# Optimization experiments

Measured on AMD Instinct MI355X. Metric: run time of the kernel, lower is better.

## Reference

```python
import jax, jax.numpy as jnp
import numpy as np

NODE_DIM = 256
OUT_DIM = 512
NUM_HEADS = 8
HEAD_DIM = 32
HID = NUM_HEADS * HEAD_DIM  # 256
N_NODES = 200000
N_GRAPHS = 2000


def _linear_init(key, fan_in, fan_out):
    lim = 1.0 / np.sqrt(fan_in)
    kw, kb = jax.random.split(key)
    w = jax.random.uniform(kw, (fan_in, fan_out), minval=-lim, maxval=lim, dtype=jnp.float32)
    b = jax.random.uniform(kb, (fan_out,), minval=-lim, maxval=lim, dtype=jnp.float32)
    return w, b


def setup_inputs() -> dict:
    key = jax.random.key(0)
    ks = jax.random.split(key, 16)
    inp = {}
    inp["node_embeddings"] = jax.random.normal(ks[0], (N_NODES, NODE_DIM), dtype=jnp.float32)
    inp["node_to_graph_id"] = jnp.sort(jax.random.randint(ks[1], (N_NODES,), 0, N_GRAPHS)).astype(jnp.int64)
    inp["num_graphs"] = N_GRAPHS
    # weighted_mean pooler params
    inp["wm_score_w1"], inp["wm_score_b1"] = _linear_init(ks[2], NODE_DIM, HID)
    inp["wm_score_w2"], inp["wm_score_b2"] = _linear_init(ks[3], HID, NUM_HEADS)
    inp["wm_val_w1"], inp["wm_val_b1"] = _linear_init(ks[4], NODE_DIM, HID)
    inp["wm_val_w2"], inp["wm_val_b2"] = _linear_init(ks[5], HID, NUM_HEADS * HEAD_DIM)
    inp["wm_comb_w"] = _linear_init(ks[6], NUM_HEADS * HEAD_DIM, OUT_DIM)[0]
    # weighted_sum pooler params
    inp["ws_score_w1"], inp["ws_score_b1"] = _linear_init(ks[7], NODE_DIM, HID)
    inp["ws_score_w2"], inp["ws_score_b2"] = _linear_init(ks[8], HID, NUM_HEADS)
    inp["ws_val_w1"], inp["ws_val_b1"] = _linear_init(ks[9], NODE_DIM, HID)
    inp["ws_val_w2"], inp["ws_val_b2"] = _linear_init(ks[10], HID, NUM_HEADS * HEAD_DIM)
    inp["ws_comb_w"] = _linear_init(ks[11], NUM_HEADS * HEAD_DIM, OUT_DIM)[0]
    # max pooler + final combination
    inp["mx_comb_w"] = _linear_init(ks[12], NODE_DIM, OUT_DIM)[0]
    inp["final_w"] = _linear_init(ks[13], 3 * OUT_DIM, OUT_DIM)[0]
    return inp


def _mlp(x, w1, b1, w2, b2):
    return jax.nn.relu(x @ w1 + b1) @ w2 + b2


def _scatter_softmax(scores, seg, num_graphs):
    # scores: [N, H]; softmax over nodes within each graph, per head
    m = jax.ops.segment_max(scores, seg, num_segments=num_graphs)
    m = jnp.where(jnp.isfinite(m), m, 0.0)  # empty graphs
    e = jnp.exp(scores - m[seg])
    s = jax.ops.segment_sum(e, seg, num_segments=num_graphs)
    return e / s[seg]


def _multihead_readout(x, seg, num_graphs, sw1, sb1, sw2, sb2, vw1, vb1, vw2, vb2, cw, weighted_mean):
    scores = _mlp(x, sw1, sb1, sw2, sb2)                       # [N, heads]
    if weighted_mean:
        weights = _scatter_softmax(scores, seg, num_graphs)
    else:
        weights = jax.nn.sigmoid(scores)
    values = _mlp(x, vw1, vb1, vw2, vb2).reshape(-1, NUM_HEADS, HEAD_DIM)
    weighted = (weights[:, :, None] * values).reshape(-1, NUM_HEADS * HEAD_DIM)
    per_graph = jax.ops.segment_sum(weighted, seg, num_segments=num_graphs)
    return per_graph @ cw


def reference(node_embeddings, node_to_graph_id, num_graphs,
              wm_score_w1, wm_score_b1, wm_score_w2, wm_score_b2,
              wm_val_w1, wm_val_b1, wm_val_w2, wm_val_b2, wm_comb_w,
              ws_score_w1, ws_score_b1, ws_score_w2, ws_score_b2,
              ws_val_w1, ws_val_b1, ws_val_w2, ws_val_b2, ws_comb_w,
              mx_comb_w, final_w):
    seg = node_to_graph_id.astype(jnp.int32)
    mean_repr = _multihead_readout(node_embeddings, seg, num_graphs,
                                   wm_score_w1, wm_score_b1, wm_score_w2, wm_score_b2,
                                   wm_val_w1, wm_val_b1, wm_val_w2, wm_val_b2, wm_comb_w, True)
    sum_repr = _multihead_readout(node_embeddings, seg, num_graphs,
                                  ws_score_w1, ws_score_b1, ws_score_w2, ws_score_b2,
                                  ws_val_w1, ws_val_b1, ws_val_w2, ws_val_b2, ws_comb_w, False)
    pg_max = jax.ops.segment_max(node_embeddings, seg, num_segments=num_graphs)
    pg_max = jnp.where(jnp.isfinite(pg_max), pg_max, 0.0)  # torch_scatter zeros empty segments
    max_repr = pg_max @ mx_comb_w
    raw = jnp.concatenate([mean_repr, sum_repr, max_repr], axis=1)  # [G, 3*out_dim]
    return jax.nn.relu(raw) @ final_w
```

## Files before the change

### kernel.cpp

```cpp
#include <hip/hip_runtime.h>
#include <hip/hip_bf16.h>

typedef __bf16 bf16_t;
typedef __bf16 bf16x8 __attribute__((ext_vector_type(8)));
typedef float  f32x4  __attribute__((ext_vector_type(4)));

#define MFMA16(a, b, c) __builtin_amdgcn_mfma_f32_16x16x32_bf16((a), (b), (c), 0, 0, 0)

#define ROWS 32

__device__ __forceinline__ int gray(int row) { return (row ^ (row >> 1)) & 7; }
__device__ __forceinline__ int swz256(int row, int col) {
    return row * 256 + ((((col >> 3) ^ gray(row)) << 3) | (col & 7));
}

__device__ __forceinline__ bf16x8 cvt8(float4 a, float4 b) {
    bf16x8 o;
    o[0] = (bf16_t)a.x; o[1] = (bf16_t)a.y; o[2] = (bf16_t)a.z; o[3] = (bf16_t)a.w;
    o[4] = (bf16_t)b.x; o[5] = (bf16_t)b.y; o[6] = (bf16_t)b.z; o[7] = (bf16_t)b.w;
    return o;
}

__device__ __forceinline__ unsigned enc_max(float x) {
    unsigned b = __float_as_uint(x);
    return (b & 0x80000000u) ? ~b : (b | 0x80000000u);
}
__device__ __forceinline__ float dec_max(unsigned e) {
    if (e == 0u) return 0.0f;
    return (e & 0x80000000u) ? __uint_as_float(e ^ 0x80000000u) : __uint_as_float(~e);
}

__device__ __forceinline__ void gemm256p(const bf16_t* __restrict__ As,
                                         const bf16_t* __restrict__ Wk,
                                         f32x4 acc[2][2], int w, int l) {
    const int l15 = l & 15, hi = l >> 4;
#pragma unroll
    for (int mt = 0; mt < 2; ++mt)
#pragma unroll
        for (int j = 0; j < 2; ++j) acc[mt][j] = (f32x4){0.f, 0.f, 0.f, 0.f};

    const bf16_t* wb = Wk + ((size_t)hi * 256 + w * 32 + l15) * 8;

    bf16x8 b0[3], b1[3];
    bf16x8 a[2][2];
    b0[0] = *(const bf16x8*)(wb);
    b1[0] = *(const bf16x8*)(wb + 128);
    b0[1] = *(const bf16x8*)(wb + 8192);
    b1[1] = *(const bf16x8*)(wb + 8192 + 128);
#pragma unroll
    for (int mt = 0; mt < 2; ++mt) {
        const int row = mt * 16 + l15;
        a[0][mt] = *(const bf16x8*)(As + row * 256 + (hi ^ gray(row)) * 8);
    }

#pragma unroll
    for (int kt = 0; kt < 8; ++kt) {
        const int cur = kt % 3, nx2 = (kt + 2) % 3;
        if (kt + 2 < 8) {
            b0[nx2] = *(const bf16x8*)(wb + (kt + 2) * 8192);
            b1[nx2] = *(const bf16x8*)(wb + (kt + 2) * 8192 + 128);
        }
        if (kt + 1 < 8) {
#pragma unroll
            for (int mt = 0; mt < 2; ++mt) {
                const int row = mt * 16 + l15;
                a[(kt + 1) & 1][mt] =
                    *(const bf16x8*)(As + row * 256 + (((kt + 1) * 4 + hi) ^ gray(row)) * 8);
            }
        }
#pragma unroll
        for (int mt = 0; mt < 2; ++mt) {
            acc[mt][0] = MFMA16(a[kt & 1][mt], b0[cur], acc[mt][0]);
            acc[mt][1] = MFMA16(a[kt & 1][mt], b1[cur], acc[mt][1]);
        }
    }
}

__device__ __forceinline__ void write_h(f32x4 acc[2][2], const float* __restrict__ bias,
                                        bool relu, bf16_t* __restrict__ dst, int w, int l) {
    const int l15 = l & 15, hi = l >> 4;
#pragma unroll
    for (int j = 0; j < 2; ++j) {
        const int col = w * 32 + j * 16 + l15;
        const float bv = bias[col];
#pragma unroll
        for (int mt = 0; mt < 2; ++mt)
#pragma unroll
            for (int r = 0; r < 4; ++r) {
                const int row = mt * 16 + hi * 4 + r;
                float v = acc[mt][j][r] + bv;
                if (relu) v = fmaxf(v, 0.f);
                dst[swz256(row, col)] = (bf16_t)v;
            }
    }
}

__device__ __forceinline__ void gemm_score(const bf16_t* __restrict__ As,
                                           const bf16_t* __restrict__ W2k,
                                           const float* __restrict__ b2,
                                           float* __restrict__ ssc, int coloff, int w, int l) {
    if (w >= 2) return;
    const int l15 = l & 15, hi = l >> 4;
    const int row = w * 16 + l15;
    const bf16_t* wb = W2k + ((size_t)hi * 16 + l15) * 8;
    bf16x8 b[3];
    b[0] = *(const bf16x8*)(wb);
    b[1] = *(const bf16x8*)(wb + 512);
    f32x4 acc = (f32x4){0.f, 0.f, 0.f, 0.f};
#pragma unroll
    for (int kt = 0; kt < 8; ++kt) {
        const int cur = kt % 3, nx2 = (kt + 2) % 3;
        if (kt + 2 < 8) b[nx2] = *(const bf16x8*)(wb + (kt + 2) * 512);
        bf16x8 a = *(const bf16x8*)(As + row * 256 + ((kt * 4 + hi) ^ gray(row)) * 8);
        acc = MFMA16(a, b[cur], acc);
    }
    if (l15 < 8) {
        const float bv = b2[l15];
#pragma unroll
        for (int r = 0; r < 4; ++r) {
            const int orow = w * 16 + hi * 4 + r;
            ssc[orow * 16 + coloff + l15] = acc[r] + bv;
        }
    }
}

template <bool WM>
__device__ __forceinline__ void reduce_seg(const bf16_t* __restrict__ sh,
                                           const float* __restrict__ ssc,
                                           const bf16_t* __restrict__ sx,
                                           const int* __restrict__ sseg,
                                           float* __restrict__ num, float* __restrict__ den,
                                           unsigned* __restrict__ pmax, int G) {
    const int col = threadIdx.x & 255;
    const int rbeg = (threadIdx.x >> 8) * 16;
    float av = 0.f, ad = 0.f;
    unsigned am = 0u;
    int gcur = sseg[rbeg];
    for (int r = rbeg; r < rbeg + 16; ++r) {
        const int g = sseg[r];
        if (g != gcur) {
            if ((unsigned)gcur < (unsigned)G) {
                atomicAdd(&num[(size_t)gcur * 256 + col], av);
                if (WM) {
                    if (col < 8) atomicAdd(&den[(size_t)gcur * 8 + col], ad);
                    atomicMax(&pmax[(size_t)gcur * 256 + col], am);
                }
            }
            av = 0.f; ad = 0.f; am = 0u; gcur = g;
        }
        const int si = swz256(r, col);
        const float v = (float)sh[si];
        const float wgt = ssc[r * 16 + (WM ? 0 : 8) + (col >> 5)];
        av += wgt * v;
        if (WM) {
            if (col < 8) ad += ssc[r * 16 + col];
            am = max(am, enc_max((float)sx[si]));
        }
    }
    if ((unsigned)gcur < (unsigned)G) {
        atomicAdd(&num[(size_t)gcur * 256 + col], av);
        if (WM) {
            if (col < 8) atomicAdd(&den[(size_t)gcur * 8 + col], ad);
            atomicMax(&pmax[(size_t)gcur * 256 + col], am);
        }
    }
}

__global__ __launch_bounds__(512, 3) void node_kernel(
    const float* __restrict__ X, const int* __restrict__ seg,
    const bf16_t* __restrict__ wt_sw1_wm, const bf16_t* __restrict__ wt_sw2_wm,
    const bf16_t* __restrict__ wt_vw1_wm, const bf16_t* __restrict__ wt_vw2_wm,
    const bf16_t* __restrict__ wt_sw1_ws, const bf16_t* __restrict__ wt_sw2_ws,
    const bf16_t* __restrict__ wt_vw1_ws, const bf16_t* __restrict__ wt_vw2_ws,
    const float* __restrict__ b_sw1_wm, const float* __restrict__ b_sw2_wm,
    const float* __restrict__ b_vw1_wm, const float* __restrict__ b_vw2_wm,
    const float* __restrict__ b_sw1_ws, const float* __restrict__ b_sw2_ws,
    const float* __restrict__ b_vw1_ws, const float* __restrict__ b_vw2_ws,
    float* __restrict__ num_wm, float* __restrict__ den_wm,
    float* __restrict__ acc_ws, unsigned* __restrict__ pmax, int N, int G) {
    __shared__ __align__(16) bf16_t sx[ROWS * 256];
    __shared__ __align__(16) bf16_t sh[ROWS * 256];
    __shared__ float ssc[ROWS * 16];
    __shared__ int sseg[ROWS];

    const int tid = threadIdx.x;
    const int w = tid >> 6, l = tid & 63;
    const int r0 = blockIdx.x * ROWS;

#pragma unroll
    for (int i = 0; i < 2; ++i) {
        const int cid = tid + i * 512;
        const int row = cid >> 5, ch = cid & 31;
        bf16x8 o;
        if (r0 + row < N) {
            const float4* gp = (const float4*)(X + (size_t)(r0 + row) * 256 + ch * 8);
            o = cvt8(gp[0], gp[1]);
        } else {
            for (int j = 0; j < 8; ++j) o[j] = (bf16_t)0.f;
        }
        *(bf16x8*)(sx + row * 256 + (ch ^ gray(row)) * 8) = o;
    }
    if (tid < ROWS) sseg[tid] = (r0 + tid < N) ? seg[r0 + tid] : -1;
    __syncthreads();

    f32x4 acc[2][2];

    gemm256p(sx, wt_sw1_wm, acc, w, l);
    write_h(acc, b_sw1_wm, true, sh, w, l);
    __syncthreads();
    gemm_score(sh, wt_sw2_wm, b_sw2_wm, ssc, 0, w, l);
    __syncthreads();

    gemm256p(sx, wt_sw1_ws, acc, w, l);
    write_h(acc, b_sw1_ws, true, sh, w, l);
    __syncthreads();
    gemm_score(sh, wt_sw2_ws, b_sw2_ws, ssc, 8, w, l);
    __syncthreads();

    {
        const float v = ssc[tid];
        ssc[tid] = ((tid & 15) < 8) ? __expf(v) : 1.f / (1.f + __expf(-v));
    }
    __syncthreads();

    gemm256p(sx, wt_vw1_wm, acc, w, l);
    write_h(acc, b_vw1_wm, true, sh, w, l);
    __syncthreads();
    gemm256p(sh, wt_vw2_wm, acc, w, l);
    __syncthreads();
    write_h(acc, b_vw2_wm, false, sh, w, l);
    __syncthreads();
    reduce_seg<true>(sh, ssc, sx, sseg, num_wm, den_wm, pmax, G);
    __syncthreads();

    gemm256p(sx, wt_vw1_ws, acc, w, l);
    write_h(acc, b_vw1_ws, true, sh, w, l);
    __syncthreads();
    gemm256p(sh, wt_vw2_ws, acc, w, l);
    __syncthreads();
    write_h(acc, b_vw2_ws, false, sx, w, l);
    __syncthreads();
    reduce_seg<false>(sx, ssc, sx, sseg, acc_ws, nullptr, nullptr, G);
}

__global__ __launch_bounds__(256, 2) void graph_kernel(
    const float* __restrict__ num_wm, const float* __restrict__ den_wm,
    const float* __restrict__ acc_ws, const unsigned* __restrict__ pmax,
    const bf16_t* __restrict__ wt_comb_wm, const bf16_t* __restrict__ wt_comb_ws,
    const bf16_t* __restrict__ wt_comb_mx, const bf16_t* __restrict__ wt_final,
    float* __restrict__ out, int G) {
    __shared__ __align__(16) bf16_t sa[16 * 256];
    __shared__ __align__(16) bf16_t sraw[16 * 1536];

    const int tid = threadIdx.x, w = tid >> 6, l = tid & 63;
    const int l15 = l & 15, hi = l >> 4;
    const int g0 = blockIdx.x * 16;

    for (int src = 0; src < 3; ++src) {
#pragma unroll
        for (int i = 0; i < 2; ++i) {
            const int cid = tid + i * 256;
            const int row = cid >> 5, ch = cid & 31;
            const int g = g0 + row;
            bf16x8 o;
            if (g < G) {
                if (src == 0) {
                    const float4* np = (const float4*)(num_wm + (size_t)g * 256 + ch * 8);
                    float4 v0 = np[0], v1 = np[1];
                    const float d = den_wm[(size_t)g * 8 + (ch >> 2)];
                    const float rd = (d > 0.f) ? 1.f / d : 0.f;
                    o[0] = (bf16_t)(v0.x * rd); o[1] = (bf16_t)(v0.y * rd);
                    o[2] = (bf16_t)(v0.z * rd); o[3] = (bf16_t)(v0.w * rd);
                    o[4] = (bf16_t)(v1.x * rd); o[5] = (bf16_t)(v1.y * rd);
                    o[6] = (bf16_t)(v1.z * rd); o[7] = (bf16_t)(v1.w * rd);
                } else if (src == 1) {
                    const float4* np = (const float4*)(acc_ws + (size_t)g * 256 + ch * 8);
                    o = cvt8(np[0], np[1]);
                } else {
                    const unsigned* mp = pmax + (size_t)g * 256 + ch * 8;
#pragma unroll
                    for (int j = 0; j < 8; ++j) o[j] = (bf16_t)dec_max(mp[j]);
                }
            } else {
                for (int j = 0; j < 8; ++j) o[j] = (bf16_t)0.f;
            }
            *(bf16x8*)(sa + row * 256 + (ch ^ gray(row)) * 8) = o;
        }
        __syncthreads();

        const bf16_t* Wt = (src == 0) ? wt_comb_wm : ((src == 1) ? wt_comb_ws : wt_comb_mx);
        bf16x8 a[8];
#pragma unroll
        for (int kt = 0; kt < 8; ++kt)
            a[kt] = *(const bf16x8*)(sa + l15 * 256 + ((kt * 4 + hi) ^ gray(l15)) * 8);
        f32x4 acc[8];
#pragma unroll
        for (int j = 0; j < 8; ++j) acc[j] = (f32x4){0.f, 0.f, 0.f, 0.f};
#pragma unroll
        for (int kt = 0; kt < 8; ++kt) {
            bf16x8 b[8];
#pragma unroll
            for (int j = 0; j < 8; ++j) {
                const int ncol = (w * 8 + j) * 16 + l15;
                b[j] = *(const bf16x8*)(Wt + ((size_t)(kt * 4 + hi) * 512 + ncol) * 8);
            }
#pragma unroll
            for (int j = 0; j < 8; ++j) acc[j] = MFMA16(a[kt], b[j], acc[j]);
        }
#pragma unroll
        for (int j = 0; j < 8; ++j) {
            const int col = src * 512 + (w * 8 + j) * 16 + l15;
#pragma unroll
            for (int r = 0; r < 4; ++r) {
                const int row = hi * 4 + r;
                const float v = fmaxf(acc[j][r], 0.f);
                sraw[row * 1536 + ((((col >> 3) ^ gray(row)) << 3) | (col & 7))] = (bf16_t)v;
            }
        }
        __syncthreads();
    }

    f32x4 facc[8];
#pragma unroll
    for (int j = 0; j < 8; ++j) facc[j] = (f32x4){0.f, 0.f, 0.f, 0.f};
    for (int kt = 0; kt < 48; ++kt) {
        bf16x8 a = *(const bf16x8*)(sraw + l15 * 1536 + ((kt * 4 + hi) ^ gray(l15)) * 8);
#pragma unroll
        for (int j = 0; j < 8; ++j) {
            const int ncol = (w * 8 + j) * 16 + l15;
            bf16x8 b = *(const bf16x8*)(wt_final + ((size_t)(kt * 4 + hi) * 512 + ncol) * 8);
            facc[j] = MFMA16(a, b, facc[j]);
        }
    }
#pragma unroll
    for (int j = 0; j < 8; ++j) {
        const int col = (w * 8 + j) * 16 + l15;
#pragma unroll
        for (int r = 0; r < 4; ++r) {
            const int row = hi * 4 + r;
            if (g0 + row < G) out[(size_t)(g0 + row) * 512 + col] = facc[j][r];
        }
    }
}

struct PrepTab {
    const float* src[12];
    bf16_t* dst[12];
    int K[12], Nn[12], Nout[12];
    int base[13];
};

__global__ void prep_all(PrepTab t) {
    const int idx = blockIdx.x * blockDim.x + threadIdx.x;
    if (idx >= t.base[12]) return;
    int i = 0;
#pragma unroll
    for (int s = 0; s < 12; ++s)
        if (idx >= t.base[s + 1]) i = s + 1;
    const int local = idx - t.base[i];
    const int j = local & 7;
    const int rest = local >> 3;
    const int n = rest % t.Nout[i];
    const int kc = rest / t.Nout[i];
    const int k = kc * 8 + j;
    const float v = (n < t.Nn[i]) ? t.src[i][(size_t)k * t.Nn[i] + n] : 0.f;
    t.dst[i][local] = (bf16_t)v;
}

extern "C" void kernel_launch(void* const* d_in, const int* in_sizes, int n_in,
                              void* d_out, int out_size, void* d_ws, size_t ws_size,
                              hipStream_t stream) {
    const float* X = (const float*)d_in[0];
    const int* seg = (const int*)d_in[1];
    const int N = in_sizes[1];
    const int G = out_size / 512;

    float* num_wm = (float*)d_ws;
    float* acc_ws = num_wm + (size_t)G * 256;
    float* den_wm = acc_ws + (size_t)G * 256;
    unsigned* pmax = (unsigned*)(den_wm + (size_t)G * 8);
    bf16_t* wt = (bf16_t*)(pmax + (size_t)G * 256);

    bf16_t* wt_sw1_wm = wt;
    bf16_t* wt_sw2_wm = wt_sw1_wm + 65536;
    bf16_t* wt_vw1_wm = wt_sw2_wm + 4096;
    bf16_t* wt_vw2_wm = wt_vw1_wm + 65536;
    bf16_t* wt_sw1_ws = wt_vw2_wm + 65536;
    bf16_t* wt_sw2_ws = wt_sw1_ws + 65536;
    bf16_t* wt_vw1_ws = wt_sw2_ws + 4096;
    bf16_t* wt_vw2_ws = wt_vw1_ws + 65536;
    bf16_t* wt_comb_wm = wt_vw2_ws + 65536;
    bf16_t* wt_comb_ws = wt_comb_wm + 131072;
    bf16_t* wt_comb_mx = wt_comb_ws + 131072;
    bf16_t* wt_final = wt_comb_mx + 131072;

    const size_t accum_bytes = ((size_t)G * 256 * 3 + (size_t)G * 8) * 4;
    hipMemsetAsync(d_ws, 0, accum_bytes, stream);

    struct TT { int srcIdx; bf16_t* dst; int K, Nn, Nout; };
    const TT tt[12] = {
        {3,  wt_sw1_wm, 256, 256, 256},  {5,  wt_sw2_wm, 256, 8,   16},
        {7,  wt_vw1_wm, 256, 256, 256},  {9,  wt_vw2_wm, 256, 256, 256},
        {12, wt_sw1_ws, 256, 256, 256},  {14, wt_sw2_ws, 256, 8,   16},
        {16, wt_vw1_ws, 256, 256, 256},  {18, wt_vw2_ws, 256, 256, 256},
        {11, wt_comb_wm, 256, 512, 512}, {20, wt_comb_ws, 256, 512, 512},
        {21, wt_comb_mx, 256, 512, 512}, {22, wt_final, 1536, 512, 512},
    };
    PrepTab pt;
    int base = 0;
    for (int i = 0; i < 12; ++i) {
        pt.src[i] = (const float*)d_in[tt[i].srcIdx];
        pt.dst[i] = tt[i].dst;
        pt.K[i] = tt[i].K; pt.Nn[i] = tt[i].Nn; pt.Nout[i] = tt[i].Nout;
        pt.base[i] = base;
        base += tt[i].K * tt[i].Nout;
    }
    pt.base[12] = base;
    prep_all<<<(base + 255) / 256, 256, 0, stream>>>(pt);

    const int nb = (N + ROWS - 1) / ROWS;
    node_kernel<<<nb, 512, 0, stream>>>(
        X, seg,
        wt_sw1_wm, wt_sw2_wm, wt_vw1_wm, wt_vw2_wm,
        wt_sw1_ws, wt_sw2_ws, wt_vw1_ws, wt_vw2_ws,
        (const float*)d_in[4], (const float*)d_in[6], (const float*)d_in[8], (const float*)d_in[10],
        (const float*)d_in[13], (const float*)d_in[15], (const float*)d_in[17], (const float*)d_in[19],
        num_wm, den_wm, acc_ws, pmax, N, G);

    const int gb = (G + 15) / 16;
    graph_kernel<<<gb, 256, 0, stream>>>(num_wm, den_wm, acc_ws, pmax,
                                         wt_comb_wm, wt_comb_ws, wt_comb_mx, wt_final,
                                         (float*)d_out, G);
}
```

Baseline: 325.6 us.

## Fuse value-MLP epilogue with segment reduction in registers and enlarge row tile

Replaces the write-to-LDS-then-reduce path for the value MLP outputs with a register-level reduction: each lane scales its MFMA accumulators by the softmax/sigmoid weight, sums per graph id via masked accumulation and cross-lane shuffles, and issues atomics directly. The rows per block grow from 32 to 48, so each block amortises its weight loads over more rows. The max pooling and the denominator accumulation are split into separate simpler passes. This removes two barriers and an LDS round-trip per pooler. In exchange, per-thread register pressure rises under a 3-blocks-per-CU launch bound, and the per-graph loop with shuffles runs once for every distinct graph id in the tile.

```diff
diff --git a/kernel.cpp b/kernel.cpp
--- a/kernel.cpp
+++ b/kernel.cpp
@@ -7,7 +7,7 @@
 
 #define MFMA16(a, b, c) __builtin_amdgcn_mfma_f32_16x16x32_bf16((a), (b), (c), 0, 0, 0)
 
-#define ROWS 32
+#define ROWS 48
 
 __device__ __forceinline__ int gray(int row) { return (row ^ (row >> 1)) & 7; }
 __device__ __forceinline__ int swz256(int row, int col) {
@@ -32,23 +32,23 @@
 
 __device__ __forceinline__ void gemm256p(const bf16_t* __restrict__ As,
                                          const bf16_t* __restrict__ Wk,
-                                         f32x4 acc[2][2], int w, int l) {
+                                         f32x4 acc[3][2], int w, int l) {
     const int l15 = l & 15, hi = l >> 4;
 #pragma unroll
-    for (int mt = 0; mt < 2; ++mt)
+    for (int mt = 0; mt < 3; ++mt)
 #pragma unroll
         for (int j = 0; j < 2; ++j) acc[mt][j] = (f32x4){0.f, 0.f, 0.f, 0.f};
 
     const bf16_t* wb = Wk + ((size_t)hi * 256 + w * 32 + l15) * 8;
 
     bf16x8 b0[3], b1[3];
-    bf16x8 a[2][2];
+    bf16x8 a[2][3];
     b0[0] = *(const bf16x8*)(wb);
     b1[0] = *(const bf16x8*)(wb + 128);
     b0[1] = *(const bf16x8*)(wb + 8192);
     b1[1] = *(const bf16x8*)(wb + 8192 + 128);
 #pragma unroll
-    for (int mt = 0; mt < 2; ++mt) {
+    for (int mt = 0; mt < 3; ++mt) {
         const int row = mt * 16 + l15;
         a[0][mt] = *(const bf16x8*)(As + row * 256 + (hi ^ gray(row)) * 8);
     }
@@ -62,36 +62,83 @@
         }
         if (kt + 1 < 8) {
 #pragma unroll
-            for (int mt = 0; mt < 2; ++mt) {
+            for (int mt = 0; mt < 3; ++mt) {
                 const int row = mt * 16 + l15;
                 a[(kt + 1) & 1][mt] =
                     *(const bf16x8*)(As + row * 256 + (((kt + 1) * 4 + hi) ^ gray(row)) * 8);
             }
         }
 #pragma unroll
-        for (int mt = 0; mt < 2; ++mt) {
+        for (int mt = 0; mt < 3; ++mt) {
             acc[mt][0] = MFMA16(a[kt & 1][mt], b0[cur], acc[mt][0]);
             acc[mt][1] = MFMA16(a[kt & 1][mt], b1[cur], acc[mt][1]);
         }
     }
 }
 
-__device__ __forceinline__ void write_h(f32x4 acc[2][2], const float* __restrict__ bias,
-                                        bool relu, bf16_t* __restrict__ dst, int w, int l) {
+__device__ __forceinline__ void write_h(f32x4 acc[3][2], const float* __restrict__ bias,
+                                        bf16_t* __restrict__ dst, int w, int l) {
     const int l15 = l & 15, hi = l >> 4;
 #pragma unroll
     for (int j = 0; j < 2; ++j) {
         const int col = w * 32 + j * 16 + l15;
         const float bv = bias[col];
 #pragma unroll
-        for (int mt = 0; mt < 2; ++mt)
+        for (int mt = 0; mt < 3; ++mt)
 #pragma unroll
             for (int r = 0; r < 4; ++r) {
                 const int row = mt * 16 + hi * 4 + r;
-                float v = acc[mt][j][r] + bv;
-                if (relu) v = fmaxf(v, 0.f);
-                dst[swz256(row, col)] = (bf16_t)v;
-            }
+                dst[swz256(row, col)] = (bf16_t)fmaxf(acc[mt][j][r] + bv, 0.f);
+            }
+    }
+}
+
+template <bool WM>
+__device__ __forceinline__ void fused_reduce(f32x4 acc[3][2],
+                                             const float* __restrict__ bias,
+                                             const float* __restrict__ ssc,
+                                             const int* __restrict__ sseg,
+                                             float* __restrict__ num,
+                                             int nv, int G, int w, int l) {
+    const int l15 = l & 15, hi = l >> 4;
+    int rseg[3][4];
+#pragma unroll
+    for (int mt = 0; mt < 3; ++mt)
+#pragma unroll
+        for (int r = 0; r < 4; ++r) rseg[mt][r] = sseg[mt * 16 + hi * 4 + r];
+
+    float val[2][3][4];
+#pragma unroll
+    for (int j = 0; j < 2; ++j) {
+        const int col = w * 32 + j * 16 + l15;
+        const int off = (WM ? 0 : 8) + (col >> 5);
+        const float bv = bias[col];
+#pragma unroll
+        for (int mt = 0; mt < 3; ++mt)
+#pragma unroll
+            for (int r = 0; r < 4; ++r) {
+                const int row = mt * 16 + hi * 4 + r;
+                val[j][mt][r] = (acc[mt][j][r] + bv) * ssc[row * 16 + off];
+            }
+    }
+
+    const int g0 = sseg[0], g1 = sseg[nv - 1];
+    for (int g = g0; g <= g1; ++g) {
+#pragma unroll
+        for (int j = 0; j < 2; ++j) {
+            float s = 0.f;
+#pragma unroll
+            for (int mt = 0; mt < 3; ++mt)
+#pragma unroll
+                for (int r = 0; r < 4; ++r)
+                    s += (rseg[mt][r] == g) ? val[j][mt][r] : 0.f;
+            s += __shfl_xor(s, 16);
+            s += __shfl_xor(s, 32);
+            if (hi == 0 && (unsigned)g < (unsigned)G) {
+                const int col = w * 32 + j * 16 + l15;
+                atomicAdd(&num[(size_t)g * 256 + col], s);
+            }
+        }
     }
 }
 
@@ -99,7 +146,7 @@
                                            const bf16_t* __restrict__ W2k,
                                            const float* __restrict__ b2,
                                            float* __restrict__ ssc, int coloff, int w, int l) {
-    if (w >= 2) return;
+    if (w >= 3) return;
     const int l15 = l & 15, hi = l >> 4;
     const int row = w * 16 + l15;
     const bf16_t* wb = W2k + ((size_t)hi * 16 + l15) * 8;
@@ -124,46 +171,24 @@
     }
 }
 
-template <bool WM>
-__device__ __forceinline__ void reduce_seg(const bf16_t* __restrict__ sh,
-                                           const float* __restrict__ ssc,
-                                           const bf16_t* __restrict__ sx,
-                                           const int* __restrict__ sseg,
-                                           float* __restrict__ num, float* __restrict__ den,
-                                           unsigned* __restrict__ pmax, int G) {
+__device__ __forceinline__ void max_seg(const bf16_t* __restrict__ sx,
+                                        const int* __restrict__ sseg,
+                                        unsigned* __restrict__ pmax, int G) {
     const int col = threadIdx.x & 255;
-    const int rbeg = (threadIdx.x >> 8) * 16;
-    float av = 0.f, ad = 0.f;
+    const int rbeg = (threadIdx.x >> 8) * 24;
     unsigned am = 0u;
     int gcur = sseg[rbeg];
-    for (int r = rbeg; r < rbeg + 16; ++r) {
+    for (int r = rbeg; r < rbeg + 24; ++r) {
         const int g = sseg[r];
         if (g != gcur) {
-            if ((unsigned)gcur < (unsigned)G) {
-                atomicAdd(&num[(size_t)gcur * 256 + col], av);
-                if (WM) {
-                    if (col < 8) atomicAdd(&den[(size_t)gcur * 8 + col], ad);
-                    atomicMax(&pmax[(size_t)gcur * 256 + col], am);
-                }
-            }
-            av = 0.f; ad = 0.f; am = 0u; gcur = g;
-        }
-        const int si = swz256(r, col);
-        const float v = (float)sh[si];
-        const float wgt = ssc[r * 16 + (WM ? 0 : 8) + (col >> 5)];
-        av += wgt * v;
-        if (WM) {
-            if (col < 8) ad += ssc[r * 16 + col];
-            am = max(am, enc_max((float)sx[si]));
-        }
-    }
-    if ((unsigned)gcur < (unsigned)G) {
-        atomicAdd(&num[(size_t)gcur * 256 + col], av);
-        if (WM) {
-            if (col < 8) atomicAdd(&den[(size_t)gcur * 8 + col], ad);
-            atomicMax(&pmax[(size_t)gcur * 256 + col], am);
-        }
-    }
+            if ((unsigned)gcur < (unsigned)G)
+                atomicMax(&pmax[(size_t)gcur * 256 + col], am);
+            am = 0u; gcur = g;
+        }
+        am = max(am, enc_max((float)sx[swz256(r, col)]));
+    }
+    if ((unsigned)gcur < (unsigned)G)
+        atomicMax(&pmax[(size_t)gcur * 256 + col], am);
 }
 
 __global__ __launch_bounds__(512, 3) void node_kernel(
@@ -186,9 +211,10 @@
     const int tid = threadIdx.x;
     const int w = tid >> 6, l = tid & 63;
     const int r0 = blockIdx.x * ROWS;
-
-#pragma unroll
-    for (int i = 0; i < 2; ++i) {
+    const int nv = min(ROWS, N - r0);
+
+#pragma unroll
+    for (int i = 0; i < 3; ++i) {
         const int cid = tid + i * 512;
         const int row = cid >> 5, ch = cid & 31;
         bf16x8 o;
@@ -203,44 +229,50 @@
     if (tid < ROWS) sseg[tid] = (r0 + tid < N) ? seg[r0 + tid] : -1;
     __syncthreads();
 
-    f32x4 acc[2][2];
+    f32x4 acc[3][2];
 
     gemm256p(sx, wt_sw1_wm, acc, w, l);
-    write_h(acc, b_sw1_wm, true, sh, w, l);
+    write_h(acc, b_sw1_wm, sh, w, l);
     __syncthreads();
     gemm_score(sh, wt_sw2_wm, b_sw2_wm, ssc, 0, w, l);
     __syncthreads();
 
     gemm256p(sx, wt_sw1_ws, acc, w, l);
-    write_h(acc, b_sw1_ws, true, sh, w, l);
+    write_h(acc, b_sw1_ws, sh, w, l);
     __syncthreads();
     gemm_score(sh, wt_sw2_ws, b_sw2_ws, ssc, 8, w, l);
     __syncthreads();
 
-    {
-        const float v = ssc[tid];
-        ssc[tid] = ((tid & 15) < 8) ? __expf(v) : 1.f / (1.f + __expf(-v));
+#pragma unroll
+    for (int i = 0; i < 2; ++i) {
+        const int idx = tid + i * 512;
+        if (idx < ROWS * 16) {
+            const float v = ssc[idx];
+            ssc[idx] = ((idx & 15) < 8) ? __expf(v) : 1.f / (1.f + __expf(-v));
+        }
     }
     __syncthreads();
 
     gemm256p(sx, wt_vw1_wm, acc, w, l);
-    write_h(acc, b_vw1_wm, true, sh, w, l);
+    write_h(acc, b_vw1_wm, sh, w, l);
     __syncthreads();
     gemm256p(sh, wt_vw2_wm, acc, w, l);
-    __syncthreads();
-    write_h(acc, b_vw2_wm, false, sh, w, l);
-    __syncthreads();
-    reduce_seg<true>(sh, ssc, sx, sseg, num_wm, den_wm, pmax, G);
+    fused_reduce<true>(acc, b_vw2_wm, ssc, sseg, num_wm, nv, G, w, l);
+    if (tid < ROWS * 8) {
+        const int row = tid >> 3, h = tid & 7;
+        const int g = sseg[row];
+        if ((unsigned)g < (unsigned)G)
+            atomicAdd(&den_wm[(size_t)g * 8 + h], ssc[row * 16 + h]);
+    }
     __syncthreads();
 
     gemm256p(sx, wt_vw1_ws, acc, w, l);
-    write_h(acc, b_vw1_ws, true, sh, w, l);
+    write_h(acc, b_vw1_ws, sh, w, l);
     __syncthreads();
     gemm256p(sh, wt_vw2_ws, acc, w, l);
-    __syncthreads();
-    write_h(acc, b_vw2_ws, false, sx, w, l);
-    __syncthreads();
-    reduce_seg<false>(sx, ssc, sx, sseg, acc_ws, nullptr, nullptr, G);
+    fused_reduce<false>(acc, b_vw2_ws, ssc, sseg, acc_ws, nv, G, w, l);
+
+    max_seg(sx, sseg, pmax, G);
 }
 
 __global__ __launch_bounds__(256, 2) void graph_kernel(
```

New measurement: 381.0 us. 1.17x slower.
